# Optimization experiments

Hardware: AMD Instinct MI355X
Metric: run time of the kernel (lower is better)

Reference implementation:

```python
import jax, jax.numpy as jnp
import numpy as np
from jax import lax

D = 512        # datapathSize (= slow-net hidden size = embedding size)
H = 20         # nonlinearAfterSlowHiddenSize
V = 32000      # softmaxOutputHeadSize = xEmbeddingsNum
T = 1024       # sequence length (number of sequential fast-weight updates)


def setup_inputs() -> dict:
    key = jax.random.key(0)
    ks = jax.random.split(key, 12)
    inp = {}
    inp["tokens"] = jax.random.randint(ks[0], (T,), 0, V)
    inp["targets"] = jax.random.randint(ks[1], (T,), 0, V)
    # learned parameters
    inp["embed"] = jax.random.normal(ks[2], (V, D), dtype=jnp.float32)
    # fastWeightsInit = rand(D,D) * (1/D)
    inp["fw_init"] = jax.random.uniform(ks[3], (D, D), dtype=jnp.float32) * (1.0 / D)
    inp["eta"] = jnp.array(1.0, dtype=jnp.float32)
    inp["wa"] = jax.random.normal(ks[4], (D, D), dtype=jnp.float32) * 0.05
    inp["wb"] = jax.random.normal(ks[5], (D, D), dtype=jnp.float32) * 0.05
    # nonlinearAfterSlow: Linear(D,H) -> selu -> Linear(H,D); stored as (in,out)
    lim_a = 1.0 / np.sqrt(D)
    inp["mlp_aw"] = jax.random.uniform(ks[6], (D, H), dtype=jnp.float32, minval=-lim_a, maxval=lim_a)
    inp["mlp_ab"] = jax.random.uniform(ks[7], (H,), dtype=jnp.float32, minval=-lim_a, maxval=lim_a)
    lim_b = 1.0 / np.sqrt(H)
    inp["mlp_bw"] = jax.random.uniform(ks[8], (H, D), dtype=jnp.float32, minval=-lim_b, maxval=lim_b)
    inp["mlp_bb"] = jax.random.uniform(ks[9], (D,), dtype=jnp.float32, minval=-lim_b, maxval=lim_b)
    # logit head Linear(D, V)
    inp["head_w"] = jax.random.uniform(ks[10], (D, V), dtype=jnp.float32, minval=-lim_a, maxval=lim_a)
    inp["head_b"] = jax.random.uniform(ks[11], (V,), dtype=jnp.float32, minval=-lim_a, maxval=lim_a)
    return inp


def reference(tokens, targets, embed, fw_init, eta, wa, wb,
              mlp_aw, mlp_ab, mlp_bw, mlp_bb, head_w, head_b):
    xs = embed[tokens]  # [T, D]

    def step(fw, x):
        # SlowNetB.forwardAndUpdate for one token
        z0 = x @ wa                      # [D]
        z1 = x @ wb                      # [D]
        fw_new = jnp.tanh(fw + eta * jnp.outer(z0, z1))  # [D, D]
        y = x @ fw_new                   # [D]
        return fw_new, y

    _, ys = lax.scan(step, fw_init, xs)  # ys: [T, D]

    # NonlinearLayer (batched over T)
    h = jax.nn.selu(ys @ mlp_aw + mlp_ab) @ mlp_bw + mlp_bb  # [T, D]
    mixed = 0.5 * h + 0.5 * xs
    logits = mixed @ head_w + head_b     # [T, V]

    logp = jax.nn.log_softmax(logits, axis=-1)
    loss = -jnp.mean(jnp.take_along_axis(logp, targets[:, None], axis=1))
    return logits, loss
```

## Files before the change

### kernel.cpp

```cpp
#include <hip/hip_runtime.h>

#define D 512
#define H 20
#define V 32000
#define T 1024
#define NT2 500

typedef unsigned int uint;
typedef __attribute__((ext_vector_type(8))) short short8;
typedef __attribute__((ext_vector_type(4))) float floatx4;

#define CC 2.8853900817779268f
#define M2C -5.7707801635558537f

__device__ __forceinline__ unsigned short f2bf(float f) {
    unsigned u = __builtin_bit_cast(unsigned, f);
    u += 0x7fffu + ((u >> 16) & 1u);
    return (unsigned short)(u >> 16);
}

template <int CTRL>
__device__ __forceinline__ float dpp_add(float v) {
    int x = __builtin_amdgcn_update_dpp(0, __builtin_bit_cast(int, v), CTRL, 0xf, 0xf, true);
    return v + __builtin_bit_cast(float, x);
}
template <int CTRL>
__device__ __forceinline__ float dpp_max(float v) {
    int x = __builtin_amdgcn_update_dpp(0, __builtin_bit_cast(int, v), CTRL, 0xf, 0xf, true);
    return fmaxf(v, __builtin_bit_cast(float, x));
}
__device__ __forceinline__ float reduce16(float v) {
    v = dpp_add<0xB1>(v);
    v = dpp_add<0x4E>(v);
    v = dpp_add<0x141>(v);
    v = dpp_add<0x140>(v);
    return v;
}
__device__ __forceinline__ float reduce16max(float v) {
    v = dpp_max<0xB1>(v);
    v = dpp_max<0x4E>(v);
    v = dpp_max<0x141>(v);
    v = dpp_max<0x140>(v);
    return v;
}

__global__ __launch_bounds__(256) void gather_kernel(const int* __restrict__ tokens,
                                                     const float* __restrict__ embed,
                                                     float* __restrict__ xs,
                                                     float* __restrict__ loss_acc) {
    int idx = blockIdx.x * 256 + threadIdx.x;
    if (idx == 0) *loss_acc = 0.f;
    int row = idx >> 7;
    int c   = idx & 127;
    float4 v = ((const float4*)(embed + (long)tokens[row] * D))[c];
    ((float4*)xs)[idx] = v;
}

__global__ __launch_bounds__(256) void zgemm_kernel(const float* __restrict__ xs,
                                                    const float* __restrict__ wa,
                                                    const float* __restrict__ wb,
                                                    const float* __restrict__ eta_p,
                                                    float* __restrict__ z0,
                                                    float* __restrict__ z1) {
    __shared__ float Xs[16 * 36];
    __shared__ float Ws[16 * 68];
    const int tid = threadIdx.x;
    const int n0 = blockIdx.x * 64, m0 = blockIdx.y * 32;
    const float* Wm = blockIdx.z ? wb : wa;
    float* Z = blockIdx.z ? z1 : z0;
    const float sc = blockIdx.z ? 1.0f : (*eta_p) * CC;
    const int tx = tid & 15, ty = tid >> 4;
    const int xr = tid >> 3, xk = (tid & 7) * 2;
    const int wr = tid >> 4, wc = (tid & 15) * 4;
    float acc[2][4] = {};
    for (int k0 = 0; k0 < D; k0 += 16) {
        float2 xv = *(const float2*)(xs + (m0 + xr) * D + k0 + xk);
        float4 wv = *(const float4*)(Wm + (k0 + wr) * D + n0 + wc);
        Xs[(xk + 0) * 36 + xr] = xv.x;
        Xs[(xk + 1) * 36 + xr] = xv.y;
        *(float4*)(Ws + wr * 68 + wc) = wv;
        __syncthreads();
#pragma unroll
        for (int k = 0; k < 16; k++) {
            float a0 = Xs[k * 36 + 2 * ty];
            float a1 = Xs[k * 36 + 2 * ty + 1];
            float4 b = *(const float4*)(Ws + k * 68 + tx * 4);
            float bv[4] = {b.x, b.y, b.z, b.w};
#pragma unroll
            for (int c = 0; c < 4; c++) {
                acc[0][c] = __builtin_fmaf(a0, bv[c], acc[0][c]);
                acc[1][c] = __builtin_fmaf(a1, bv[c], acc[1][c]);
            }
        }
        __syncthreads();
    }
    float4 v0 = {sc * acc[0][0], sc * acc[0][1], sc * acc[0][2], sc * acc[0][3]};
    float4 v1 = {sc * acc[1][0], sc * acc[1][1], sc * acc[1][2], sc * acc[1][3]};
    *(float4*)(Z + (m0 + 2 * ty + 0) * D + n0 + tx * 4) = v0;
    *(float4*)(Z + (m0 + 2 * ty + 1) * D + n0 + tx * 4) = v1;
}

#define LOADC(B, cb)                                                          \
    {                                                                         \
        _Pragma("unroll")                                                     \
        for (int c = 0; c < 8; c++) {                                         \
            const int tr = ((cb) * 8 + c) * D;                                \
            za##B[c] = *(const float2*)(z0 + tr + i0);                        \
            xa##B[c] = *(const float2*)(xs + tr + i0);                        \
            ez##B[c] = z1[tr + j];                                            \
        }                                                                     \
        __builtin_amdgcn_sched_barrier(0);                                    \
    }

#define COMPUTE(B, cb)                                                        \
    {                                                                         \
        float p[8];                                                           \
        _Pragma("unroll")                                                     \
        for (int c = 0; c < 8; c++) {                                         \
            float e = ez##B[c];                                               \
            float a0 = __builtin_amdgcn_exp2f(__builtin_fmaf(e, za##B[c].x, g0)); \
            float a1 = __builtin_amdgcn_exp2f(__builtin_fmaf(e, za##B[c].y, g1)); \
            float r0 = __builtin_amdgcn_rcpf(a0 + 1.0f);                      \
            float r1 = __builtin_amdgcn_rcpf(a1 + 1.0f);                      \
            g0 = __builtin_fmaf(M2C, r0, CC);                                 \
            g1 = __builtin_fmaf(M2C, r1, CC);                                 \
            p[c] = xa##B[c].x * g0 + xa##B[c].y * g1;                         \
        }                                                                     \
        _Pragma("unroll")                                                     \
        for (int c = 0; c < 8; c++) {                                         \
            float v = reduce16(p[c]);                                         \
            v += __shfl_xor(v, 16, 64);                                       \
            v += __shfl_xor(v, 32, 64);                                       \
            p[c] = v;                                                         \
        }                                                                     \
        if (lane == 0) {                                                      \
            _Pragma("unroll")                                                 \
            for (int c = 0; c < 8; c++)                                       \
                __builtin_nontemporal_store(p[c], yp + ((cb) * 8 + c) * D);   \
        }                                                                     \
        __builtin_amdgcn_sched_barrier(0);                                    \
    }

__global__ __launch_bounds__(64) void scan_kernel(const float* __restrict__ z0,
                                                  const float* __restrict__ z1,
                                                  const float* __restrict__ xs,
                                                  const float* __restrict__ fw_init,
                                                  float* __restrict__ ypart) {
    const int lane = threadIdx.x;
    const int bid = blockIdx.x;
    const int j = bid & 511;
    const int q = bid >> 9;
    const int i0 = q * 128 + 2 * lane;
    float g0 = CC * fw_init[(long)i0 * D + j];
    float g1 = CC * fw_init[(long)(i0 + 1) * D + j];
    float* yp = ypart + (long)q * T * D + j;

    float2 za0[8], xa0[8], za1[8], xa1[8], za2[8], xa2[8], za3[8], xa3[8];
    float  ez0[8], ez1[8], ez2[8], ez3[8];

    LOADC(0, 0); LOADC(1, 1); LOADC(2, 2);
    for (int i = 0; i < 128; i += 4) {
        LOADC(3, i + 3);
        COMPUTE(0, i);
        LOADC(0, i + 4);
        COMPUTE(1, i + 1);
        LOADC(1, i + 5);
        COMPUTE(2, i + 2);
        LOADC(2, i + 6);
        COMPUTE(3, i + 3);
    }
}

__global__ __launch_bounds__(256) void mlp_fused_kernel(const float* __restrict__ ypart,
                                                        const float* __restrict__ xs,
                                                        const float* __restrict__ Aw,
                                                        const float* __restrict__ Ab,
                                                        const float* __restrict__ Bw,
                                                        const float* __restrict__ Bb,
                                                        unsigned short* __restrict__ mixed) {
    const int t = blockIdx.x, tid = threadIdx.x;
    __shared__ float y_lds[D];
    __shared__ float h_lds[H];
    const float INVC = 0.34657359027997264f;
#pragma unroll
    for (int s = 0; s < 2; s++) {
        int d = s * 256 + tid;
        float v = 0.f;
#pragma unroll
        for (int qq = 0; qq < 4; qq++)
            v += __builtin_nontemporal_load(ypart + ((long)qq * T + t) * D + d);
        y_lds[d] = v * INVC;
    }
    __syncthreads();
    const int w = tid >> 6, lane = tid & 63;
    float yv[8];
#pragma unroll
    for (int k = 0; k < 8; k++) yv[k] = y_lds[k * 64 + lane];
#pragma unroll
    for (int u = 0; u < 5; u++) {
        const int jj = w * 5 + u;
        float a = 0.f;
#pragma unroll
        for (int k = 0; k < 8; k++)
            a = __builtin_fmaf(yv[k], Aw[(k * 64 + lane) * H + jj], a);
        a = reduce16(a);
        a += __shfl_xor(a, 16, 64);
        a += __shfl_xor(a, 32, 64);
        if (lane == 0) {
            a += Ab[jj];
            const float sc = 1.0507009873554805f, al = 1.6732632423543772f;
            h_lds[jj] = a > 0.f ? sc * a : sc * al * (__expf(a) - 1.f);
        }
    }
    __syncthreads();
#pragma unroll
    for (int s = 0; s < 2; s++) {
        int d = s * 256 + tid;
        float o = Bb[d];
#pragma unroll
        for (int jj = 0; jj < H; jj++) o = __builtin_fmaf(h_lds[jj], Bw[jj * D + d], o);
        int gi = t * D + d;
        mixed[gi] = f2bf(0.5f * o + 0.5f * xs[gi]);
    }
}

__global__ __launch_bounds__(256) void convert_wt_kernel(const float* __restrict__ head_w,
                                                         unsigned short* __restrict__ wt) {
    __shared__ float tile[64 * 68];
    const int n0 = blockIdx.x * 64, k0 = blockIdx.y * 64;
    const int tid = threadIdx.x;
#pragma unroll
    for (int s = 0; s < 4; s++) {
        int idx4 = s * 256 + tid;
        int r = idx4 >> 4, c4 = idx4 & 15;
        float4 v = *(const float4*)(head_w + (long)(k0 + r) * V + n0 + c4 * 4);
        *(float4*)(tile + r * 68 + c4 * 4) = v;
    }
    __syncthreads();
    const int rr = tid >> 2;
    const int cq = tid & 3;
    uint u[8];
#pragma unroll
    for (int p = 0; p < 8; p++) {
        float a = tile[(cq * 16 + p * 2 + 0) * 68 + rr];
        float b = tile[(cq * 16 + p * 2 + 1) * 68 + rr];
        u[p] = (uint)f2bf(a) | ((uint)f2bf(b) << 16);
    }
    unsigned short* ob = wt + (long)(n0 + rr) * D + k0 + cq * 16;
    uint4 v0 = {u[0], u[1], u[2], u[3]};
    uint4 v1 = {u[4], u[5], u[6], u[7]};
    *(uint4*)ob = v0;
    *((uint4*)ob + 1) = v1;
}

__global__ __launch_bounds__(256) void head_gemm_kernel(const unsigned short* __restrict__ A,
                                                        const unsigned short* __restrict__ Bt,
                                                        const float* __restrict__ bias,
                                                        float* __restrict__ C,
                                                        float* __restrict__ pm,
                                                        float* __restrict__ ps) {
    __shared__ unsigned short As[128 * 64];
    __shared__ unsigned short Bs[128 * 64];
    const int tid = threadIdx.x;
    const int bid = blockIdx.x;
    const int xcd = bid & 7;
    const int mt = (bid >> 3) & 7;
    const int nt = (bid >> 6) * 8 + xcd;
    if (nt >= V / 128) return;
    const int m0 = mt * 128, n0 = nt * 128;
    const int wave = tid >> 6, lane = tid & 63;
    const int wm = wave >> 1, wn = wave & 1;
    const int quad = lane >> 4, l15 = lane & 15;
    floatx4 acc[4][4] = {};
    for (int k0 = 0; k0 < D; k0 += 64) {
#pragma unroll
        for (int s = 0; s < 4; s++) {
            int idx = s * 256 + tid;
            int row = idx >> 3, slot = idx & 7;
            int gch = slot ^ (row & 7);
            const unsigned short* ga = A + (long)(m0 + row) * D + k0 + gch * 8;
            __builtin_amdgcn_global_load_lds(
                (const __attribute__((address_space(1))) unsigned int*)ga,
                (__attribute__((address_space(3))) unsigned int*)(As + idx * 8), 16, 0, 0);
            const unsigned short* gb = Bt + (long)(n0 + row) * D + k0 + gch * 8;
            __builtin_amdgcn_global_load_lds(
                (const __attribute__((address_space(1))) unsigned int*)gb,
                (__attribute__((address_space(3))) unsigned int*)(Bs + idx * 8), 16, 0, 0);
        }
        __syncthreads();
#pragma unroll
        for (int ks = 0; ks < 2; ks++) {
            short8 af[4], bfr[4];
            int q = ks * 4 + quad;
#pragma unroll
            for (int f = 0; f < 4; f++) {
                int ar = wm * 64 + f * 16 + l15;
                af[f] = *(const short8*)(As + ar * 64 + ((q ^ (ar & 7)) * 8));
                int br = wn * 64 + f * 16 + l15;
                bfr[f] = *(const short8*)(Bs + br * 64 + ((q ^ (br & 7)) * 8));
            }
#pragma unroll
            for (int fr = 0; fr < 4; fr++)
#pragma unroll
                for (int fc = 0; fc < 4; fc++)
                    acc[fr][fc] = __builtin_amdgcn_mfma_f32_16x16x32_bf16(af[fr], bfr[fc],
                                                                          acc[fr][fc], 0, 0, 0);
        }
        __syncthreads();
    }
    float bv[4];
#pragma unroll
    for (int fc = 0; fc < 4; fc++) bv[fc] = bias[n0 + wn * 64 + fc * 16 + l15];
#pragma unroll
    for (int fr = 0; fr < 4; fr++) {
        int mr = m0 + wm * 64 + fr * 16 + quad * 4;
#pragma unroll
        for (int r = 0; r < 4; r++) {
            float v[4];
#pragma unroll
            for (int fc = 0; fc < 4; fc++) {
                v[fc] = acc[fr][fc][r] + bv[fc];
                C[(long)(mr + r) * V + n0 + wn * 64 + fc * 16 + l15] = v[fc];
            }
            float mx = fmaxf(fmaxf(v[0], v[1]), fmaxf(v[2], v[3]));
            mx = reduce16max(mx);
            float sv = __expf(v[0] - mx) + __expf(v[1] - mx)
                     + __expf(v[2] - mx) + __expf(v[3] - mx);
            sv = reduce16(sv);
            if (l15 == 0) {
                long row = mr + r;
                pm[row * NT2 + nt * 2 + wn] = mx;
                ps[row * NT2 + nt * 2 + wn] = sv;
            }
        }
    }
}

__device__ __forceinline__ void lse_comb(float& m, float& s, float m2, float s2) {
    float M = fmaxf(m, m2);
    s = s * __expf(m - M) + s2 * __expf(m2 - M);
    m = M;
}

__global__ __launch_bounds__(256) void loss_rows_kernel(const float* __restrict__ pm,
                                                        const float* __restrict__ ps,
                                                        const float* __restrict__ logits,
                                                        const int* __restrict__ targets,
                                                        float* __restrict__ loss_acc) {
    const int t = blockIdx.x, tid = threadIdx.x;
    float m = -INFINITY, s = 0.f;
    for (int i = tid; i < NT2; i += 256)
        lse_comb(m, s, pm[(long)t * NT2 + i], ps[(long)t * NT2 + i]);
#pragma unroll
    for (int msk = 1; msk <= 32; msk <<= 1) {
        float m2 = __shfl_xor(m, msk, 64);
        float s2 = __shfl_xor(s, msk, 64);
        lse_comb(m, s, m2, s2);
    }
    __shared__ float sm[4], ss[4];
    if ((tid & 63) == 0) { sm[tid >> 6] = m; ss[tid >> 6] = s; }
    __syncthreads();
    if (tid == 0) {
        float M = sm[0], S = ss[0];
#pragma unroll
        for (int w = 1; w < 4; w++) lse_comb(M, S, sm[w], ss[w]);
        float lse = M + __logf(S);
        float lt = logits[(long)t * V + targets[t]];
        atomicAdd(loss_acc, (lse - lt) * (1.0f / (float)T));
    }
}

extern "C" void kernel_launch(void* const* d_in, const int* in_sizes, int n_in,
                              void* d_out, int out_size, void* d_ws, size_t ws_size,
                              hipStream_t stream) {
    const int*   tokens  = (const int*)d_in[0];
    const int*   targets = (const int*)d_in[1];
    const float* embed   = (const float*)d_in[2];
    const float* fw_init = (const float*)d_in[3];
    const float* eta     = (const float*)d_in[4];
    const float* wa      = (const float*)d_in[5];
    const float* wb      = (const float*)d_in[6];
    const float* mlp_aw  = (const float*)d_in[7];
    const float* mlp_ab  = (const float*)d_in[8];
    const float* mlp_bw  = (const float*)d_in[9];
    const float* mlp_bb  = (const float*)d_in[10];
    const float* head_w  = (const float*)d_in[11];
    const float* head_b  = (const float*)d_in[12];
    float* out = (float*)d_out;
    float* loss_acc = out + (long)T * V;

    char* ws = (char*)d_ws;
    float*          xs      = (float*)(ws + 0);
    float*          z0      = (float*)(ws + 2097152);
    float*          z1      = (float*)(ws + 4194304);
    float*          ypart   = (float*)(ws + 6291456);
    unsigned short* wt      = (unsigned short*)(ws + 2097152);
    unsigned short* mixed   = (unsigned short*)(ws + 35651584);
    float*          pm      = (float*)(ws + 36700160);
    float*          psum    = (float*)(ws + 38797312);

    gather_kernel<<<(T * D / 4) / 256, 256, 0, stream>>>(tokens, embed, xs, loss_acc);
    zgemm_kernel<<<dim3(D / 64, T / 32, 2), 256, 0, stream>>>(xs, wa, wb, eta, z0, z1);
    scan_kernel<<<2048, 64, 0, stream>>>(z0, z1, xs, fw_init, ypart);
    mlp_fused_kernel<<<T, 256, 0, stream>>>(ypart, xs, mlp_aw, mlp_ab, mlp_bw, mlp_bb, mixed);
    convert_wt_kernel<<<dim3(V / 64, D / 64), 256, 0, stream>>>(head_w, wt);
    head_gemm_kernel<<<2048, 256, 0, stream>>>(mixed, wt, head_b, out, pm, psum);
    loss_rows_kernel<<<T, 256, 0, stream>>>(pm, psum, out, targets, loss_acc);
}
```

Baseline: 549.8 us.

## Split scan output into sixteen per-group partials and drop cross-group shuffles

The scan kernel now reduces each step's dot product only within 16-lane groups. It writes 16 partial sums per (t, j) instead of shuffling across the full wave, and the MLP kernel sums those 16 partials. The scan pipeline changes from a 4-deep to a 2-deep register double buffer, and the sched_barrier fences are removed so the compiler can interleave loads and math more freely. The head GEMM also drops its XCD-aware block remapping, and the workspace layout is reshuffled to fit the larger partial buffer. The trade-off is four times more partial-sum traffic to write and read back, in exchange for fewer cross-lane ops in the latency-bound scan.

```diff
diff --git a/kernel.cpp b/kernel.cpp
--- a/kernel.cpp
+++ b/kernel.cpp
@@ -5,6 +5,7 @@
 #define V 32000
 #define T 1024
 #define NT2 500
+#define NPART 16
 
 typedef unsigned int uint;
 typedef __attribute__((ext_vector_type(8))) short short8;
@@ -100,19 +101,18 @@
     *(float4*)(Z + (m0 + 2 * ty + 1) * D + n0 + tx * 4) = v1;
 }
 
-#define LOADC(B, cb)                                                          \
+#define LOADC(B, tbase)                                                       \
     {                                                                         \
         _Pragma("unroll")                                                     \
         for (int c = 0; c < 8; c++) {                                         \
-            const int tr = ((cb) * 8 + c) * D;                                \
+            const int tr = ((tbase) + c) * D;                                 \
             za##B[c] = *(const float2*)(z0 + tr + i0);                        \
             xa##B[c] = *(const float2*)(xs + tr + i0);                        \
             ez##B[c] = z1[tr + j];                                            \
         }                                                                     \
-        __builtin_amdgcn_sched_barrier(0);                                    \
-    }
-
-#define COMPUTE(B, cb)                                                        \
+    }
+
+#define COMPUTE(B, tbase)                                                     \
     {                                                                         \
         float p[8];                                                           \
         _Pragma("unroll")                                                     \
@@ -124,21 +124,14 @@
             float r1 = __builtin_amdgcn_rcpf(a1 + 1.0f);                      \
             g0 = __builtin_fmaf(M2C, r0, CC);                                 \
             g1 = __builtin_fmaf(M2C, r1, CC);                                 \
-            p[c] = xa##B[c].x * g0 + xa##B[c].y * g1;                         \
+            p[c] = __builtin_fmaf(xa##B[c].y, g1, xa##B[c].x * g0);           \
         }                                                                     \
         _Pragma("unroll")                                                     \
-        for (int c = 0; c < 8; c++) {                                         \
-            float v = reduce16(p[c]);                                         \
-            v += __shfl_xor(v, 16, 64);                                       \
-            v += __shfl_xor(v, 32, 64);                                       \
-            p[c] = v;                                                         \
+        for (int c = 0; c < 8; c++) p[c] = reduce16(p[c]);                    \
+        if ((lane & 15) == 0) {                                               \
+            _Pragma("unroll")                                                 \
+            for (int c = 0; c < 8; c++) yp[((tbase) + c) * D] = p[c];         \
         }                                                                     \
-        if (lane == 0) {                                                      \
-            _Pragma("unroll")                                                 \
-            for (int c = 0; c < 8; c++)                                       \
-                __builtin_nontemporal_store(p[c], yp + ((cb) * 8 + c) * D);   \
-        }                                                                     \
-        __builtin_amdgcn_sched_barrier(0);                                    \
     }
 
 __global__ __launch_bounds__(64) void scan_kernel(const float* __restrict__ z0,
@@ -153,21 +146,17 @@
     const int i0 = q * 128 + 2 * lane;
     float g0 = CC * fw_init[(long)i0 * D + j];
     float g1 = CC * fw_init[(long)(i0 + 1) * D + j];
-    float* yp = ypart + (long)q * T * D + j;
-
-    float2 za0[8], xa0[8], za1[8], xa1[8], za2[8], xa2[8], za3[8], xa3[8];
-    float  ez0[8], ez1[8], ez2[8], ez3[8];
-
-    LOADC(0, 0); LOADC(1, 1); LOADC(2, 2);
-    for (int i = 0; i < 128; i += 4) {
-        LOADC(3, i + 3);
-        COMPUTE(0, i);
-        LOADC(0, i + 4);
-        COMPUTE(1, i + 1);
-        LOADC(1, i + 5);
-        COMPUTE(2, i + 2);
-        LOADC(2, i + 6);
-        COMPUTE(3, i + 3);
+    float* yp = ypart + ((long)(q * 4 + (lane >> 4)) * T) * D + j;
+
+    float2 zaA[8], xaA[8], zaB[8], xaB[8];
+    float  ezA[8], ezB[8];
+
+    LOADC(A, 0);
+    for (int t0 = 0; t0 < T; t0 += 16) {
+        LOADC(B, t0 + 8);
+        COMPUTE(A, t0);
+        if (t0 + 16 < T) { LOADC(A, t0 + 16); }
+        COMPUTE(B, t0 + 8);
     }
 }
 
@@ -187,7 +176,7 @@
         int d = s * 256 + tid;
         float v = 0.f;
 #pragma unroll
-        for (int qq = 0; qq < 4; qq++)
+        for (int qq = 0; qq < NPART; qq++)
             v += __builtin_nontemporal_load(ypart + ((long)qq * T + t) * D + d);
         y_lds[d] = v * INVC;
     }
@@ -262,11 +251,7 @@
     __shared__ unsigned short As[128 * 64];
     __shared__ unsigned short Bs[128 * 64];
     const int tid = threadIdx.x;
-    const int bid = blockIdx.x;
-    const int xcd = bid & 7;
-    const int mt = (bid >> 3) & 7;
-    const int nt = (bid >> 6) * 8 + xcd;
-    if (nt >= V / 128) return;
+    const int mt = blockIdx.x & 7, nt = blockIdx.x >> 3;
     const int m0 = mt * 128, n0 = nt * 128;
     const int wave = tid >> 6, lane = tid & 63;
     const int wm = wave >> 1, wn = wave & 1;
@@ -395,15 +380,15 @@
     float*          z1      = (float*)(ws + 4194304);
     float*          ypart   = (float*)(ws + 6291456);
     unsigned short* wt      = (unsigned short*)(ws + 2097152);
-    unsigned short* mixed   = (unsigned short*)(ws + 35651584);
-    float*          pm      = (float*)(ws + 36700160);
-    float*          psum    = (float*)(ws + 38797312);
+    float*          pm      = (float*)(ws + 0);
+    float*          psum    = (float*)(ws + 37748736);
+    unsigned short* mixed   = (unsigned short*)(ws + 39845888);
 
     gather_kernel<<<(T * D / 4) / 256, 256, 0, stream>>>(tokens, embed, xs, loss_acc);
     zgemm_kernel<<<dim3(D / 64, T / 32, 2), 256, 0, stream>>>(xs, wa, wb, eta, z0, z1);
     scan_kernel<<<2048, 64, 0, stream>>>(z0, z1, xs, fw_init, ypart);
     mlp_fused_kernel<<<T, 256, 0, stream>>>(ypart, xs, mlp_aw, mlp_ab, mlp_bw, mlp_bb, mixed);
     convert_wt_kernel<<<dim3(V / 64, D / 64), 256, 0, stream>>>(head_w, wt);
-    head_gemm_kernel<<<2048, 256, 0, stream>>>(mixed, wt, head_b, out, pm, psum);
+    head_gemm_kernel<<<(T / 128) * (V / 128), 256, 0, stream>>>(mixed, wt, head_b, out, pm, psum);
     loss_rows_kernel<<<T, 256, 0, stream>>>(pm, psum, out, targets, loss_acc);
 }
```

After: 548.9 us. No clear change (-0.2%).
